# Kernel optimization log

Measured on AMD Instinct MI355X. Metric: run time of the kernel, lower is better.

The kernel has to match this reference:

```python
import jax, jax.numpy as jnp
import numpy as np

B, T, D, H, WIN = 4, 2048, 512, 8, 128
DK = D // H
DFF = 4 * D
LN_EPS = 1e-5


def setup_inputs() -> dict:
    key = jax.random.key(0)
    ks = jax.random.split(key, 12)
    p = lambda k, shp: jax.random.normal(k, shp, jnp.float32) * 0.02
    return {
        "x": jax.random.normal(ks[0], (B, T, D), jnp.float32),
        "pad_mask": jnp.ones((B, T), dtype=bool),
        "wq": p(ks[1], (D, D)), "bq": jnp.zeros((D,), jnp.float32),
        "wk": p(ks[2], (D, D)), "bk": jnp.zeros((D,), jnp.float32),
        "wv": p(ks[3], (D, D)), "bv": jnp.zeros((D,), jnp.float32),
        "wo": p(ks[4], (D, D)), "bo": jnp.zeros((D,), jnp.float32),
        "w1": p(ks[5], (D, DFF)), "b1": jnp.zeros((DFF,), jnp.float32),
        "w2": p(ks[6], (DFF, D)), "b2": jnp.zeros((D,), jnp.float32),
        "g1": jnp.ones((D,), jnp.float32), "be1": jnp.zeros((D,), jnp.float32),
        "g2": jnp.ones((D,), jnp.float32), "be2": jnp.zeros((D,), jnp.float32),
    }


def _ln(x, g, b):
    m = x.mean(-1, keepdims=True)
    v = ((x - m) ** 2).mean(-1, keepdims=True)
    return (x - m) * jax.lax.rsqrt(v + LN_EPS) * g + b


def reference(x, pad_mask, wq, bq, wk, bk, wv, bv, wo, bo,
              w1, b1, w2, b2, g1, be1, g2, be2):
    Bv, Tv, Dv = x.shape
    # projections -> [B, H, T, DK]
    q = (x @ wq + bq).reshape(Bv, Tv, H, DK).transpose(0, 2, 1, 3)
    k = (x @ wk + bk).reshape(Bv, Tv, H, DK).transpose(0, 2, 1, 3)
    v = (x @ wv + bv).reshape(Bv, Tv, H, DK).transpose(0, 2, 1, 3)
    idx = jnp.arange(Tv)
    dist = idx[None, :] - idx[:, None]  # q rows, k cols? matches torch: idx[None,:]-idx[:,None] with rows=q
    wmask = (dist >= 0) & (dist < WIN)  # note: dist = k - q in torch code orientation; see original
    # original: dist = idx[None,:] - idx[:,None]; window_mask[q, k] = (k - q >= 0)&(k - q < W)? No:
    # torch uses dist[q, k] = idx[None,:][q,k] - idx[:,None][q,k] = k - q, mask (dist>=0)&(dist<W)
    # so key index >= query index within window — reproduce exactly.
    mask = pad_mask[:, None, None, :] & wmask[None, None, :, :]  # [B,1,T,T]
    scores = jnp.einsum('bhqd,bhkd->bhqk', q, k) / np.float32(np.sqrt(DK))
    scores = jnp.where(mask, scores, jnp.float32(-1e9))
    attn = jax.nn.softmax(scores, axis=-1)
    o = jnp.einsum('bhqk,bhkd->bhqd', attn, v)
    o = o.transpose(0, 2, 1, 3).reshape(Bv, Tv, Dv)
    attn_out = o @ wo + bo
    x1 = _ln(x + attn_out, g1, be1)
    ff = jax.nn.relu(x1 @ w1 + b1) @ w2 + b2
    return _ln(x1 + ff, g2, be2)
```

## Files before the change

### kernel.cpp

```cpp
#include <hip/hip_runtime.h>

typedef __bf16 bf16;
typedef float  f32x4  __attribute__((ext_vector_type(4)));
typedef __bf16 bf16x8 __attribute__((ext_vector_type(8)));

#define GLOAD_LDS16(gsrc, ldst) \
  __builtin_amdgcn_global_load_lds((const __attribute__((address_space(1))) void*)(gsrc), \
                                   (__attribute__((address_space(3))) void*)(ldst), 16, 0, 0)

constexpr int Bc   = 4;
constexpr int Tc   = 2048;
constexpr int Dc   = 512;
constexpr int Hc   = 8;
constexpr int DKc  = 64;
constexpr int DFFc = 2048;
constexpr int WINc = 128;
constexpr int Mr   = Bc * Tc;
constexpr size_t MD = (size_t)Mr * Dc;

__device__ bf16  g_xb[MD];
__device__ bf16  g_wqkvT[3 * Dc * Dc];
__device__ bf16  g_woT[Dc * Dc];
__device__ bf16  g_w1T[DFFc * Dc];
__device__ bf16  g_w2T[Dc * DFFc];
__device__ float g_biasqkv[3 * Dc];
__device__ bf16  g_qkv[Mr * 3 * Dc];
__device__ bf16  g_o[MD];
__device__ bf16  g_attnp[2 * MD];
__device__ bf16  g_x1b[MD];
__device__ bf16  g_ff1[Mr * DFFc];
__device__ bf16  g_ff2p[4 * MD];

__global__ __launch_bounds__(256) void cast_x_k(const float* __restrict__ x) {
  size_t i = ((size_t)blockIdx.x * 256 + threadIdx.x) * 8;
  float4 a = *(const float4*)(x + i);
  float4 c = *(const float4*)(x + i + 4);
  bf16x8 o;
  o[0] = (bf16)a.x; o[1] = (bf16)a.y; o[2] = (bf16)a.z; o[3] = (bf16)a.w;
  o[4] = (bf16)c.x; o[5] = (bf16)c.y; o[6] = (bf16)c.z; o[7] = (bf16)c.w;
  *(bf16x8*)(g_xb + i) = o;
}

__global__ __launch_bounds__(256) void prep_k(const float* __restrict__ wq, const float* __restrict__ wk,
                                              const float* __restrict__ wv, const float* __restrict__ wo,
                                              const float* __restrict__ w1, const float* __restrict__ w2,
                                              const float* __restrict__ bq, const float* __restrict__ bk,
                                              const float* __restrict__ bv) {
  int bid = blockIdx.x;
  if (bid >= 3072) {
    int i = (bid - 3072) * 256 + threadIdx.x;
    if (i < 1536) g_biasqkv[i] = (i < 512) ? bq[i] : (i < 1024 ? bk[i - 512] : bv[i - 1024]);
    return;
  }
  const float* W; bf16* dst; int K, N, nx, ky;
  if (bid < 1024) {
    int wsel = bid >> 8, local = bid & 255;
    nx = local & 15; ky = local >> 4; K = 512; N = 512;
    switch (wsel) {
      case 0: W = wq; dst = g_wqkvT;              break;
      case 1: W = wk; dst = g_wqkvT + 512 * 512;  break;
      case 2: W = wv; dst = g_wqkvT + 1024 * 512; break;
      default:W = wo; dst = g_woT;                break;
    }
  } else if (bid < 2048) {
    int local = bid - 1024;
    nx = local & 63; ky = local >> 6; K = 512; N = 2048; W = w1; dst = g_w1T;
  } else {
    int local = bid - 2048;
    nx = local & 15; ky = local >> 4; K = 2048; N = 512; W = w2; dst = g_w2T;
  }
  __shared__ float t[32][33];
  int n0 = nx * 32, k0 = ky * 32;
  int tx = threadIdx.x & 31, ty = threadIdx.x >> 5;
  #pragma unroll
  for (int i = 0; i < 4; ++i)
    t[ty + i * 8][tx] = W[(size_t)(k0 + ty + i * 8) * N + n0 + tx];
  __syncthreads();
  #pragma unroll
  for (int i = 0; i < 4; ++i)
    dst[(size_t)(n0 + ty + i * 8) * K + k0 + tx] = (bf16)t[tx][ty + i * 8];
}

__global__ __launch_bounds__(512, 2) void gemm256_k(int which, const float* __restrict__ bias_in) {
  const bf16 *A, *BT; bf16* Cb; const float* bias;
  int N, K, Klen; bool relu = false;
  int kz = blockIdx.z;
  if (which == 0)      { A = g_xb;  BT = g_wqkvT; Cb = g_qkv; bias = g_biasqkv; N = 1536; K = 512;  Klen = 512; }
  else if (which == 2) { A = g_x1b; BT = g_w1T;   Cb = g_ff1; bias = bias_in;   N = 2048; K = 512;  Klen = 512; relu = true; }
  else                 { A = g_ff1; BT = g_w2T;   Cb = g_ff2p + (size_t)kz * MD; bias = bias_in; N = 512; K = 2048; Klen = 512; }
  if (kz) bias = nullptr;

  __shared__ __align__(16) bf16 lA2[2][256 * 64];
  __shared__ __align__(16) bf16 lB2[2][256 * 64];

  const int tid = threadIdx.x;
  const int bm = blockIdx.x, bn = blockIdx.y;
  const int w = tid >> 6, lane = tid & 63;
  const int wm = w >> 2, wn = w & 3;
  const int r = lane & 15, gg = lane >> 4;
  const int kzoff = kz * Klen;

  f32x4 acc[8][4] = {};

  const bf16* gA = A  + (size_t)(bm * 256 + (tid >> 3)) * K + kzoff + (tid & 7) * 8;
  const bf16* gB = BT + (size_t)(bn * 256 + (tid >> 3)) * K + kzoff + (tid & 7) * 8;
  const int wub = (tid >> 6) << 10;

  const int nt = Klen / 64;

  {
    char* la = (char*)&lA2[0][0] + wub;
    char* lb = (char*)&lB2[0][0] + wub;
    #pragma unroll
    for (int s = 0; s < 4; ++s) {
      GLOAD_LDS16(gA + (size_t)s * 64 * K, la + s * 8192);
      GLOAD_LDS16(gB + (size_t)s * 64 * K, lb + s * 8192);
    }
  }
  asm volatile("s_waitcnt vmcnt(0)" ::: "memory");
  __syncthreads();

  for (int t = 0; t < nt; ++t) {
    const int cur = t & 1;
    if (t + 1 < nt) {
      const int kk = (t + 1) * 64;
      char* la = (char*)&lA2[cur ^ 1][0] + wub;
      char* lb = (char*)&lB2[cur ^ 1][0] + wub;
      #pragma unroll
      for (int s = 0; s < 4; ++s) {
        GLOAD_LDS16(gA + (size_t)s * 64 * K + kk, la + s * 8192);
        GLOAD_LDS16(gB + (size_t)s * 64 * K + kk, lb + s * 8192);
      }
    }
    const bf16* la = &lA2[cur][0];
    const bf16* lb = &lB2[cur][0];
    #pragma unroll
    for (int ks = 0; ks < 2; ++ks) {
      bf16x8 bfr[4];
      #pragma unroll
      for (int ni = 0; ni < 4; ++ni)
        bfr[ni] = *(const bf16x8*)(lb + (wn * 64 + ni * 16 + r) * 64 + ks * 32 + gg * 8);
      #pragma unroll
      for (int mi = 0; mi < 8; ++mi) {
        bf16x8 af = *(const bf16x8*)(la + (wm * 128 + mi * 16 + r) * 64 + ks * 32 + gg * 8);
        #pragma unroll
        for (int ni = 0; ni < 4; ++ni)
          acc[mi][ni] = __builtin_amdgcn_mfma_f32_16x16x32_bf16(af, bfr[ni], acc[mi][ni], 0, 0, 0);
      }
    }
    asm volatile("s_waitcnt vmcnt(0)" ::: "memory");
    __syncthreads();
  }

  #pragma unroll
  for (int mi = 0; mi < 8; ++mi) {
    int row0 = bm * 256 + wm * 128 + mi * 16 + gg * 4;
    #pragma unroll
    for (int ni = 0; ni < 4; ++ni) {
      int col = bn * 256 + wn * 64 + ni * 16 + r;
      float bv = bias ? bias[col] : 0.f;
      #pragma unroll
      for (int j = 0; j < 4; ++j) {
        float v0 = acc[mi][ni][j] + bv;
        if (relu) v0 = fmaxf(v0, 0.f);
        Cb[(size_t)(row0 + j) * N + col] = (bf16)v0;
      }
    }
  }
}

__global__ __launch_bounds__(256) void gemm_k(const float* __restrict__ bias_in) {
  const bf16 *A, *BT;
  bf16* Cb;
  const float* bias;
  int N, K, Klen;
  int kz = blockIdx.z;
  { A = g_o; BT = g_woT; Cb = g_attnp + (size_t)kz * MD; bias = bias_in; N = 512; K = 512; Klen = 256; }
  if (kz) bias = nullptr;

  __shared__ __align__(16) bf16 lA[128 * 32];
  __shared__ __align__(16) bf16 lB[128 * 32];
  int tid = threadIdx.x;
  int bm = blockIdx.x, bn = blockIdx.y;
  int w = tid >> 6, lane = tid & 63;
  int wm = w >> 1, wn = w & 1;
  int r = lane & 15, gg = lane >> 4;

  f32x4 acc[4][4] = {};

  const bf16* gA = A + (size_t)(bm * 128 + (tid >> 2)) * K + (size_t)kz * Klen + (tid & 3) * 8;
  const bf16* gB = BT + (size_t)(bn * 128 + (tid >> 2)) * K + (size_t)kz * Klen + (tid & 3) * 8;
  char* lAb = (char*)lA + (tid & 0xC0) * 16;
  char* lBb = (char*)lB + (tid & 0xC0) * 16;

  for (int k0 = 0; k0 < Klen; k0 += 32) {
    GLOAD_LDS16(gA + k0,                  lAb);
    GLOAD_LDS16(gA + (size_t)64 * K + k0, lAb + 4096);
    GLOAD_LDS16(gB + k0,                  lBb);
    GLOAD_LDS16(gB + (size_t)64 * K + k0, lBb + 4096);
    asm volatile("s_waitcnt vmcnt(0)" ::: "memory");
    __syncthreads();
    bf16x8 afrag[4], bfrag[4];
    #pragma unroll
    for (int i = 0; i < 4; ++i)
      afrag[i] = *(const bf16x8*)(&lA[(wm * 64 + i * 16 + r) * 32 + gg * 8]);
    #pragma unroll
    for (int i = 0; i < 4; ++i)
      bfrag[i] = *(const bf16x8*)(&lB[(wn * 64 + i * 16 + r) * 32 + gg * 8]);
    #pragma unroll
    for (int mi = 0; mi < 4; ++mi)
      #pragma unroll
      for (int ni = 0; ni < 4; ++ni)
        acc[mi][ni] = __builtin_amdgcn_mfma_f32_16x16x32_bf16(afrag[mi], bfrag[ni], acc[mi][ni], 0, 0, 0);
    __syncthreads();
  }

  #pragma unroll
  for (int mi = 0; mi < 4; ++mi) {
    int row0 = bm * 128 + wm * 64 + mi * 16 + gg * 4;
    #pragma unroll
    for (int ni = 0; ni < 4; ++ni) {
      int col = bn * 128 + wn * 64 + ni * 16 + r;
      float bv = bias ? bias[col] : 0.f;
      #pragma unroll
      for (int j = 0; j < 4; ++j) {
        float v0 = acc[mi][ni][j] + bv;
        Cb[(size_t)(row0 + j) * N + col] = (bf16)v0;
      }
    }
  }
}

__global__ __launch_bounds__(256) void attn_k() {
  constexpr int KT = 192;
  __shared__ __align__(16) bf16 lKP[KT * 64];
  __shared__ __align__(16) bf16 lVT[64 * KT];
  int tid = threadIdx.x;
  int qt = blockIdx.x, bh = blockIdx.y;
  int b = bh >> 3, h = bh & 7;
  int q0 = qt * 64;
  int w = tid >> 6, lane = tid & 63;
  int r = lane & 15, gg = lane >> 4;

  {
    int row = tid >> 3, seg = tid & 7;
    const bf16* base = g_qkv + (size_t)b * Tc * 1536 + 512 + h * 64 + seg * 8;
    char* ldst = (char*)lKP + w * 1024;
    #pragma unroll
    for (int p = 0; p < 6; ++p) {
      int key = q0 + p * 32 + row;
      int srow = key < Tc ? key : 0;
      GLOAD_LDS16(base + (size_t)srow * 1536, ldst + p * 4096);
    }
  }
  {
    int key = tid >> 3, seg = tid & 7;
    const bf16* vbase = g_qkv + (size_t)b * Tc * 1536 + 1024 + h * 64 + seg * 8;
    #pragma unroll
    for (int p = 0; p < 6; ++p) {
      int kk = p * 32 + key;
      int gk = q0 + kk;
      int srow = gk < Tc ? gk : 0;
      bf16x8 v = *(const bf16x8*)(vbase + (size_t)srow * 1536);
      #pragma unroll
      for (int i = 0; i < 8; ++i) lVT[(seg * 8 + i) * KT + kk] = v[i];
    }
  }
  bf16x8 qf0, qf1;
  {
    int qrow = q0 + w * 16 + r;
    const bf16* qp = g_qkv + (size_t)(b * Tc + qrow) * 1536 + h * 64;
    qf0 = *(const bf16x8*)(qp + gg * 8);
    qf1 = *(const bf16x8*)(qp + 32 + gg * 8);
  }
  asm volatile("s_waitcnt vmcnt(0)" ::: "memory");
  __syncthreads();

  f32x4 s[12] = {};
  #pragma unroll
  for (int ni = 0; ni < 12; ++ni) {
    bf16x8 k0f = *(const bf16x8*)(&lKP[(ni * 16 + r) * 64 + gg * 8]);
    bf16x8 k1f = *(const bf16x8*)(&lKP[(ni * 16 + r) * 64 + 32 + gg * 8]);
    s[ni] = __builtin_amdgcn_mfma_f32_16x16x32_bf16(qf0, k0f, s[ni], 0, 0, 0);
    s[ni] = __builtin_amdgcn_mfma_f32_16x16x32_bf16(qf1, k1f, s[ni], 0, 0, 0);
  }

  float mx[4] = {-3e38f, -3e38f, -3e38f, -3e38f};
  #pragma unroll
  for (int ni = 0; ni < 12; ++ni)
    #pragma unroll
    for (int j = 0; j < 4; ++j) {
      int qloc = w * 16 + gg * 4 + j;
      int col = ni * 16 + r;
      bool valid = (col >= qloc) && (col < qloc + WINc) && (q0 + col < Tc);
      float sv = valid ? s[ni][j] * 0.125f : -3e38f;
      s[ni][j] = sv;
      mx[j] = fmaxf(mx[j], sv);
    }
  #pragma unroll
  for (int m = 1; m < 16; m <<= 1)
    #pragma unroll
    for (int j = 0; j < 4; ++j) mx[j] = fmaxf(mx[j], __shfl_xor(mx[j], m, 64));

  float sm[4] = {0.f, 0.f, 0.f, 0.f};
  #pragma unroll
  for (int ni = 0; ni < 12; ++ni)
    #pragma unroll
    for (int j = 0; j < 4; ++j) {
      float p = __expf(s[ni][j] - mx[j]);
      s[ni][j] = p;
      sm[j] += p;
    }
  #pragma unroll
  for (int m = 1; m < 16; m <<= 1)
    #pragma unroll
    for (int j = 0; j < 4; ++j) sm[j] += __shfl_xor(sm[j], m, 64);

  __syncthreads();
  #pragma unroll
  for (int ni = 0; ni < 12; ++ni)
    #pragma unroll
    for (int j = 0; j < 4; ++j)
      lKP[(w * 16 + gg * 4 + j) * KT + ni * 16 + r] = (bf16)s[ni][j];
  __syncthreads();

  f32x4 o[4] = {};
  #pragma unroll
  for (int ks = 0; ks < 6; ++ks) {
    bf16x8 pf = *(const bf16x8*)(&lKP[(w * 16 + r) * KT + ks * 32 + gg * 8]);
    #pragma unroll
    for (int nf = 0; nf < 4; ++nf) {
      bf16x8 vf = *(const bf16x8*)(&lVT[(nf * 16 + r) * KT + ks * 32 + gg * 8]);
      o[nf] = __builtin_amdgcn_mfma_f32_16x16x32_bf16(pf, vf, o[nf], 0, 0, 0);
    }
  }
  #pragma unroll
  for (int nf = 0; nf < 4; ++nf) {
    int dk = nf * 16 + r;
    #pragma unroll
    for (int j = 0; j < 4; ++j) {
      int qloc = w * 16 + gg * 4 + j;
      float ov = o[nf][j] / sm[j];
      g_o[(size_t)(b * Tc + q0 + qloc) * Dc + h * 64 + dk] = (bf16)ov;
    }
  }
}

__global__ __launch_bounds__(256) void ln_k(int which, const float* __restrict__ gw,
                                            const float* __restrict__ bw,
                                            float* __restrict__ outf_in) {
  int row = blockIdx.x * 4 + (threadIdx.x >> 6);
  int lane = threadIdx.x & 63;
  const bf16* a; const bf16* pb; int np; float* outf; bf16* outb;
  if (which == 0) { a = g_xb;  pb = g_attnp; np = 2; outf = nullptr;  outb = g_x1b; }
  else            { a = g_x1b; pb = g_ff2p;  np = 4; outf = outf_in;  outb = nullptr; }
  size_t off = (size_t)row * 512 + lane * 8;
  bf16x8 av = *(const bf16x8*)(a + off);
  float v[8];
  #pragma unroll
  for (int i = 0; i < 8; ++i) v[i] = (float)av[i];
  for (int p = 0; p < np; ++p) {
    bf16x8 t = *(const bf16x8*)(pb + (size_t)p * MD + off);
    #pragma unroll
    for (int i = 0; i < 8; ++i) v[i] += (float)t[i];
  }
  float s = 0.f;
  #pragma unroll
  for (int i = 0; i < 8; ++i) s += v[i];
  #pragma unroll
  for (int m = 1; m < 64; m <<= 1) s += __shfl_xor(s, m, 64);
  float mean = s * (1.0f / 512.0f);
  float q = 0.f;
  #pragma unroll
  for (int i = 0; i < 8; ++i) { float d = v[i] - mean; q += d * d; }
  #pragma unroll
  for (int m = 1; m < 64; m <<= 1) q += __shfl_xor(q, m, 64);
  float rstd = rsqrtf(q * (1.0f / 512.0f) + 1e-5f);
  float4 g0 = *(const float4*)(gw + lane * 8), g1v = *(const float4*)(gw + lane * 8 + 4);
  float4 e0 = *(const float4*)(bw + lane * 8), e1 = *(const float4*)(bw + lane * 8 + 4);
  float gg[8] = {g0.x, g0.y, g0.z, g0.w, g1v.x, g1v.y, g1v.z, g1v.w};
  float bb[8] = {e0.x, e0.y, e0.z, e0.w, e1.x, e1.y, e1.z, e1.w};
  float o[8];
  #pragma unroll
  for (int i = 0; i < 8; ++i) o[i] = (v[i] - mean) * rstd * gg[i] + bb[i];
  if (outf) {
    float4 o0 = {o[0], o[1], o[2], o[3]}, o1 = {o[4], o[5], o[6], o[7]};
    *(float4*)(outf + off) = o0;
    *(float4*)(outf + off + 4) = o1;
  }
  if (outb) {
    bf16x8 ob;
    #pragma unroll
    for (int i = 0; i < 8; ++i) ob[i] = (bf16)o[i];
    *(bf16x8*)(outb + off) = ob;
  }
}

extern "C" void kernel_launch(void* const* d_in, const int* in_sizes, int n_in,
                              void* d_out, int out_size, void* d_ws, size_t ws_size,
                              hipStream_t stream) {
  const float* x   = (const float*)d_in[0];
  const float* wq  = (const float*)d_in[2];
  const float* bq  = (const float*)d_in[3];
  const float* wk  = (const float*)d_in[4];
  const float* bk  = (const float*)d_in[5];
  const float* wv  = (const float*)d_in[6];
  const float* bv  = (const float*)d_in[7];
  const float* wo  = (const float*)d_in[8];
  const float* bo  = (const float*)d_in[9];
  const float* w1  = (const float*)d_in[10];
  const float* b1  = (const float*)d_in[11];
  const float* w2  = (const float*)d_in[12];
  const float* b2  = (const float*)d_in[13];
  const float* g1  = (const float*)d_in[14];
  const float* be1 = (const float*)d_in[15];
  const float* g2  = (const float*)d_in[16];
  const float* be2 = (const float*)d_in[17];
  float* out = (float*)d_out;

  cast_x_k<<<2048, 256, 0, stream>>>(x);
  prep_k<<<3078, 256, 0, stream>>>(wq, wk, wv, wo, w1, w2, bq, bk, bv);

  gemm256_k<<<dim3(32, 6, 1), 512, 0, stream>>>(0, nullptr);
  attn_k<<<dim3(32, 32), 256, 0, stream>>>();
  gemm_k<<<dim3(64, 4, 2), 256, 0, stream>>>(bo);
  ln_k<<<2048, 256, 0, stream>>>(0, g1, be1, nullptr);
  gemm256_k<<<dim3(32, 8, 1), 512, 0, stream>>>(2, b1);
  gemm256_k<<<dim3(32, 2, 4), 512, 0, stream>>>(3, b2);
  ln_k<<<2048, 256, 0, stream>>>(1, g2, be2, out);
}
```

Measured before the change: 158.4 us.

## Write V transposed from QKV GEMM and XOR-swizzle attention LDS tiles

The QKV GEMM epilogue now writes the V columns in a transposed per-head layout (g_vT, with a padded time dimension). The attention kernel can then load V^T straight into LDS with async global_load_lds, replacing the scalar per-element transpose stores. K, P and V^T tiles in LDS also use an XOR swizzle on 16-byte chunks, aimed at removing bank conflicts on the MFMA fragment reads. The cost is an extra buffer and uncoalesced 8-byte strided stores in the GEMM epilogue. The padded g_vT tail is never written, but it is only read for keys past T, which are masked out.

```diff
diff --git a/kernel.cpp b/kernel.cpp
--- a/kernel.cpp
+++ b/kernel.cpp
@@ -3,6 +3,7 @@
 typedef __bf16 bf16;
 typedef float  f32x4  __attribute__((ext_vector_type(4)));
 typedef __bf16 bf16x8 __attribute__((ext_vector_type(8)));
+typedef __bf16 bf16x4 __attribute__((ext_vector_type(4)));
 
 #define GLOAD_LDS16(gsrc, ldst) \
   __builtin_amdgcn_global_load_lds((const __attribute__((address_space(1))) void*)(gsrc), \
@@ -17,6 +18,7 @@
 constexpr int WINc = 128;
 constexpr int Mr   = Bc * Tc;
 constexpr size_t MD = (size_t)Mr * Dc;
+constexpr int TVc  = 2176;
 
 __device__ bf16  g_xb[MD];
 __device__ bf16  g_wqkvT[3 * Dc * Dc];
@@ -25,6 +27,7 @@
 __device__ bf16  g_w2T[Dc * DFFc];
 __device__ float g_biasqkv[3 * Dc];
 __device__ bf16  g_qkv[Mr * 3 * Dc];
+__device__ bf16  g_vT[(size_t)Bc * Hc * DKc * TVc];
 __device__ bf16  g_o[MD];
 __device__ bf16  g_attnp[2 * MD];
 __device__ bf16  g_x1b[MD];
@@ -152,6 +155,24 @@
     __syncthreads();
   }
 
+  if (which == 0 && bn >= 4) {
+    #pragma unroll
+    for (int mi = 0; mi < 8; ++mi) {
+      int row0 = bm * 256 + wm * 128 + mi * 16 + gg * 4;
+      int bidx = row0 >> 11, t0 = row0 & 2047;
+      #pragma unroll
+      for (int ni = 0; ni < 4; ++ni) {
+        int col = bn * 256 + wn * 64 + ni * 16 + r;
+        float bv = bias[col];
+        int vcol = col - 1024;
+        bf16x4 ov;
+        #pragma unroll
+        for (int j = 0; j < 4; ++j) ov[j] = (bf16)(acc[mi][ni][j] + bv);
+        *(bf16x4*)(g_vT + (size_t)(bidx * 512 + vcol) * TVc + t0) = ov;
+      }
+    }
+    return;
+  }
   #pragma unroll
   for (int mi = 0; mi < 8; ++mi) {
     int row0 = bm * 256 + wm * 128 + mi * 16 + gg * 4;
@@ -243,27 +264,28 @@
   int r = lane & 15, gg = lane >> 4;
 
   {
-    int row = tid >> 3, seg = tid & 7;
-    const bf16* base = g_qkv + (size_t)b * Tc * 1536 + 512 + h * 64 + seg * 8;
+    const bf16* kbase = g_qkv + (size_t)b * Tc * 1536 + 512 + h * 64;
     char* ldst = (char*)lKP + w * 1024;
     #pragma unroll
     for (int p = 0; p < 6; ++p) {
-      int key = q0 + p * 32 + row;
-      int srow = key < Tc ? key : 0;
-      GLOAD_LDS16(base + (size_t)srow * 1536, ldst + p * 4096);
+      int s = p * 256 + tid;
+      int key = s >> 3;
+      int cb = (s & 7) ^ (key & 7);
+      int gkey = q0 + key;
+      int srow = gkey < Tc ? gkey : 0;
+      GLOAD_LDS16(kbase + (size_t)srow * 1536 + cb * 8, ldst + p * 4096);
     }
   }
   {
-    int key = tid >> 3, seg = tid & 7;
-    const bf16* vbase = g_qkv + (size_t)b * Tc * 1536 + 1024 + h * 64 + seg * 8;
+    const bf16* vbase = g_vT + (size_t)(bh * 64) * TVc + q0;
+    char* ldst = (char*)lVT + w * 1024;
     #pragma unroll
     for (int p = 0; p < 6; ++p) {
-      int kk = p * 32 + key;
-      int gk = q0 + kk;
-      int srow = gk < Tc ? gk : 0;
-      bf16x8 v = *(const bf16x8*)(vbase + (size_t)srow * 1536);
-      #pragma unroll
-      for (int i = 0; i < 8; ++i) lVT[(seg * 8 + i) * KT + kk] = v[i];
+      int s = p * 256 + tid;
+      int d = s / 24;
+      int sc = s - d * 24;
+      int cb = sc ^ (d & 7);
+      GLOAD_LDS16(vbase + (size_t)d * TVc + cb * 8, ldst + p * 4096);
     }
   }
   bf16x8 qf0, qf1;
@@ -279,8 +301,10 @@
   f32x4 s[12] = {};
   #pragma unroll
   for (int ni = 0; ni < 12; ++ni) {
-    bf16x8 k0f = *(const bf16x8*)(&lKP[(ni * 16 + r) * 64 + gg * 8]);
-    bf16x8 k1f = *(const bf16x8*)(&lKP[(ni * 16 + r) * 64 + 32 + gg * 8]);
+    int key = ni * 16 + r;
+    int sw = key & 7;
+    bf16x8 k0f = *(const bf16x8*)(&lKP[key * 64 + ((gg ^ sw) << 3)]);
+    bf16x8 k1f = *(const bf16x8*)(&lKP[key * 64 + (((4 | gg) ^ sw) << 3)]);
     s[ni] = __builtin_amdgcn_mfma_f32_16x16x32_bf16(qf0, k0f, s[ni], 0, 0, 0);
     s[ni] = __builtin_amdgcn_mfma_f32_16x16x32_bf16(qf1, k1f, s[ni], 0, 0, 0);
   }
@@ -320,17 +344,23 @@
   #pragma unroll
   for (int ni = 0; ni < 12; ++ni)
     #pragma unroll
-    for (int j = 0; j < 4; ++j)
-      lKP[(w * 16 + gg * 4 + j) * KT + ni * 16 + r] = (bf16)s[ni][j];
+    for (int j = 0; j < 4; ++j) {
+      int q = w * 16 + gg * 4 + j;
+      int col = ni * 16 + r;
+      int idx = q * KT + ((((col >> 3) ^ (q & 7)) << 3) | (col & 7));
+      lKP[idx] = (bf16)s[ni][j];
+    }
   __syncthreads();
 
   f32x4 o[4] = {};
+  int swl = r & 7;
   #pragma unroll
   for (int ks = 0; ks < 6; ++ks) {
-    bf16x8 pf = *(const bf16x8*)(&lKP[(w * 16 + r) * KT + ks * 32 + gg * 8]);
+    int ch = ((ks * 4 + gg) ^ swl) << 3;
+    bf16x8 pf = *(const bf16x8*)(&lKP[(w * 16 + r) * KT + ch]);
     #pragma unroll
     for (int nf = 0; nf < 4; ++nf) {
-      bf16x8 vf = *(const bf16x8*)(&lVT[(nf * 16 + r) * KT + ks * 32 + gg * 8]);
+      bf16x8 vf = *(const bf16x8*)(&lVT[(nf * 16 + r) * KT + ch]);
       o[nf] = __builtin_amdgcn_mfma_f32_16x16x32_bf16(pf, vf, o[nf], 0, 0, 0);
     }
   }
```

Result: faster. 154.4 us (-2.5%).
